# Performance work log

Hardware: AMD Instinct MI355X
Metric: run time of the kernel (lower is better)

Reference implementation:

```python
import jax, jax.numpy as jnp
import numpy as np

N = 50000          # nodes
E = 800000         # edges (COO)
IN_CH = 128
H1, H2, OUT = 200, 100, 2   # 100*out, 50*out, out with out_channels=2
EPS = 1e-12
DROP_P = 0.1


def setup_inputs() -> dict:
    key = jax.random.key(0)
    ks = jax.random.split(key, 6)
    x = jax.random.normal(ks[0], (N, IN_CH), dtype=jnp.float32)
    edge_index = jax.random.randint(ks[1], (2, E), 0, N)
    W1 = jax.random.normal(ks[2], (IN_CH, H1), dtype=jnp.float32) / np.sqrt(IN_CH)
    W2 = jax.random.normal(ks[3], (H1, H2), dtype=jnp.float32) / np.sqrt(H1)
    W3 = jax.random.normal(ks[4], (H2, OUT), dtype=jnp.float32) / np.sqrt(H2)
    beta1 = jnp.float32(1.0)
    beta2 = jnp.float32(1.0)
    beta3 = jnp.float32(1.0)
    return dict(x=x, edge_index=edge_index, W1=W1, W2=W2, W3=W3,
                beta1=beta1, beta2=beta2, beta3=beta3)


def _agnn_layer(x, W, beta, src, dst):
    # project in -> out channels, then AGNN cosine-attention propagation
    h = x @ W                                               # [N, D]
    hn = h / jnp.maximum(jnp.linalg.norm(h, axis=-1, keepdims=True), EPS)
    a = beta * jnp.sum(hn[src] * hn[dst], axis=-1)          # [E'] edge logits
    amax = jax.ops.segment_max(a, dst, num_segments=N)      # stable segment softmax
    amax = jnp.where(jnp.isfinite(amax), amax, 0.0)
    e = jnp.exp(a - amax[dst])
    denom = jax.ops.segment_sum(e, dst, num_segments=N)
    alpha = e / jnp.maximum(denom[dst], EPS)
    return jax.ops.segment_sum(h[src] * alpha[:, None], dst, num_segments=N)


def _dropout(k, x, p=DROP_P):
    keep = jax.random.bernoulli(k, 1.0 - p, x.shape)
    return jnp.where(keep, x / (1.0 - p), 0.0)


def reference(x, edge_index, W1, W2, W3, beta1, beta2, beta3):
    src, dst = edge_index[0], edge_index[1]
    loop = jnp.arange(N)                                    # self-loops (AGNNConv default)
    src = jnp.concatenate([src, loop])
    dst = jnp.concatenate([dst, loop])
    k1, k2 = jax.random.split(jax.random.key(42))
    h = jax.nn.relu(_agnn_layer(x, W1, beta1, src, dst))
    h = _dropout(k1, h)
    h = jax.nn.relu(_agnn_layer(h, W2, beta2, src, dst))
    h = _dropout(k2, h)
    h = jax.nn.relu(_agnn_layer(h, W3, beta3, src, dst))
    return h
```

## Files before the change

kernel.cpp:

```cpp
#include <hip/hip_runtime.h>
#include <hip/hip_bf16.h>

#define NN 50000
#define NE 800000
#define TE 850000
#define EPSN 1e-12f


#define H_OFF    0ull
#define A_OFF    40000000ull
#define H3_OFF   80000000ull
#define RINV_OFF 80400000ull
#define OFFS_OFF 80600000ull
#define DEG_OFF  80800016ull
#define CURS_OFF 81000016ull
#define ESRC_OFF 81200016ull
#define CHNK_OFF 84600016ull

__host__ __device__ inline void tf20(unsigned k0, unsigned k1, unsigned& x0, unsigned& x1) {
  unsigned ks2 = k0 ^ k1 ^ 0x1BD11BDAu;
  x0 += k0; x1 += k1;
#define TFR(r) { x0 += x1; x1 = ((x1 << (r)) | (x1 >> (32 - (r)))) ^ x0; }
  TFR(13) TFR(15) TFR(26) TFR(6)
  x0 += k1;  x1 += ks2 + 1u;
  TFR(17) TFR(29) TFR(16) TFR(24)
  x0 += ks2; x1 += k0 + 2u;
  TFR(13) TFR(15) TFR(26) TFR(6)
  x0 += k0;  x1 += k1 + 3u;
  TFR(17) TFR(29) TFR(16) TFR(24)
  x0 += k1;  x1 += ks2 + 4u;
  TFR(13) TFR(15) TFR(26) TFR(6)
  x0 += ks2; x1 += k0 + 5u;
#undef TFR
}

__device__ __forceinline__ float dropf(float val, unsigned k0, unsigned k1, unsigned i) {
  unsigned x0 = 0u, x1 = i;
  tf20(k0, k1, x0, x1);
  unsigned bits = x0 ^ x1;
  float u = __uint_as_float((bits >> 9) | 0x3F800000u) - 1.0f;
  return (u < 0.9f) ? val * (1.0f / 0.9f) : 0.0f;
}

__device__ __forceinline__ float wave_sum(float x) {
  x += __shfl_xor(x, 32); x += __shfl_xor(x, 16); x += __shfl_xor(x, 8);
  x += __shfl_xor(x, 4);  x += __shfl_xor(x, 2);  x += __shfl_xor(x, 1);
  return x;
}

__global__ __launch_bounds__(256) void csr_zero_kernel(int* __restrict__ p, int n) {
  int stride = gridDim.x * 256;
  for (int i = blockIdx.x * 256 + threadIdx.x; i < n; i += stride) p[i] = 0;
}

__global__ __launch_bounds__(256) void csr_hist_kernel(const int* __restrict__ ei, int* __restrict__ deg) {
  int e = blockIdx.x * 256 + threadIdx.x;
  if (e >= TE) return;
  int d = (e < NE) ? ei[NE + e] : (e - NE);
  atomicAdd(&deg[d], 1);
}

__global__ __launch_bounds__(256) void csr_scan1_kernel(const int* __restrict__ deg,
                                                        int* __restrict__ offs,
                                                        int* __restrict__ chunk) {
  __shared__ int lds[8];
  int t = threadIdx.x;
  int base = blockIdx.x * 1024 + t * 4;
  int d[4];
#pragma unroll
  for (int j = 0; j < 4; j++) d[j] = (base + j < NN) ? deg[base + j] : 0;
  int ts = d[0] + d[1] + d[2] + d[3];
  int lane = t & 63, wave = t >> 6;
  int inc = ts;
#pragma unroll
  for (int sh = 1; sh < 64; sh <<= 1) { int u = __shfl_up(inc, sh); if (lane >= sh) inc += u; }
  if (lane == 63) lds[wave] = inc;
  __syncthreads();
  if (t == 0) { int s = 0; for (int w = 0; w < 4; w++) { int x = lds[w]; lds[w] = s; s += x; } lds[4] = s; }
  __syncthreads();
  int p = lds[wave] + inc - ts;
#pragma unroll
  for (int j = 0; j < 4; j++) { if (base + j < NN) offs[base + j] = p; p += d[j]; }
  if (t == 255) chunk[blockIdx.x] = lds[4];
}

__global__ __launch_bounds__(64) void csr_scan2_kernel(int* __restrict__ chunk) {
  int t = threadIdx.x;
  int v = (t < 49) ? chunk[t] : 0;
  int inc = v;
#pragma unroll
  for (int sh = 1; sh < 64; sh <<= 1) { int u = __shfl_up(inc, sh); if (t >= sh) inc += u; }
  if (t < 49) chunk[t] = inc - v;
}

__global__ __launch_bounds__(256) void csr_scan3_kernel(int* __restrict__ offs,
                                                        const int* __restrict__ chunk,
                                                        int* __restrict__ curs) {
  int i = blockIdx.x * 256 + threadIdx.x;
  if (i < NN) {
    int val = offs[i] + chunk[i >> 10];
    offs[i] = val;
    curs[i] = val;
  }
  if (i == 0) offs[NN] = TE;
}

__global__ __launch_bounds__(256) void csr_scatter_kernel(const int* __restrict__ ei,
                                                          int* __restrict__ curs,
                                                          int* __restrict__ esrc) {
  int e = blockIdx.x * 256 + threadIdx.x;
  if (e >= TE) return;
  int s, d;
  if (e < NE) { s = ei[e]; d = ei[NE + e]; } else { s = d = e - NE; }
  int pos = atomicAdd(&curs[d], 1);
  esrc[pos] = s;
}

template<int K, int KT, int NLP, int N>
__device__ __forceinline__ void gemm_body(const float* __restrict__ A,
                                          const float* __restrict__ W,
                                          float* __restrict__ H,
                                          float* __restrict__ RINV, int M) {
  constexpr int CPT = NLP / 4, KTP = KT + 1, NV = N / 4, QV = CPT / 4;
  __shared__ float As[128 * KTP];
  __shared__ float Ws[KT * NLP];
  const float4* A4 = (const float4*)A;
  const float4* W4 = (const float4*)W;
  const float4* Ws4 = (const float4*)Ws;

  int t = threadIdx.x, rgrp = t >> 2, cg = t & 3;
  int row0 = blockIdx.x * 128;
  float acc0[CPT], acc1[CPT];
#pragma unroll
  for (int j = 0; j < CPT; j++) { acc0[j] = 0.f; acc1[j] = 0.f; }

  for (int k0 = 0; k0 < K; k0 += KT) {
    __syncthreads();
    for (int idx = t; idx < 128 * (KT / 4); idx += 256) {
      int r = idx / (KT / 4), cq = idx - r * (KT / 4);
      int gr = row0 + r;
      float4 v = (gr < M) ? A4[(size_t)gr * (K / 4) + (k0 / 4) + cq]
                          : make_float4(0.f, 0.f, 0.f, 0.f);
      float* dst = &As[r * KTP + cq * 4];
      dst[0] = v.x; dst[1] = v.y; dst[2] = v.z; dst[3] = v.w;
    }
    for (int idx = t; idx < KT * NV; idx += 256) {
      int kk = idx / NV, cq = idx - kk * NV;
      *(float4*)&Ws[kk * NLP + cq * 4] = W4[(size_t)(k0 + kk) * NV + cq];
    }
    if (NLP > N) {
      for (int idx = t; idx < KT * ((NLP - N) / 4); idx += 256) {
        int kk = idx / ((NLP - N) / 4), cq = idx - kk * ((NLP - N) / 4);
        *(float4*)&Ws[kk * NLP + N + cq * 4] = make_float4(0.f, 0.f, 0.f, 0.f);
      }
    }
    __syncthreads();
#pragma unroll
    for (int kk = 0; kk < KT; kk++) {
      float a0 = As[(rgrp * 2) * KTP + kk];
      float a1 = As[(rgrp * 2 + 1) * KTP + kk];
#pragma unroll
      for (int q = 0; q < QV; q++) {
        float4 wv = Ws4[(kk * NLP + cg * CPT) / 4 + q];
        acc0[q * 4 + 0] = fmaf(a0, wv.x, acc0[q * 4 + 0]);
        acc0[q * 4 + 1] = fmaf(a0, wv.y, acc0[q * 4 + 1]);
        acc0[q * 4 + 2] = fmaf(a0, wv.z, acc0[q * 4 + 2]);
        acc0[q * 4 + 3] = fmaf(a0, wv.w, acc0[q * 4 + 3]);
        acc1[q * 4 + 0] = fmaf(a1, wv.x, acc1[q * 4 + 0]);
        acc1[q * 4 + 1] = fmaf(a1, wv.y, acc1[q * 4 + 1]);
        acc1[q * 4 + 2] = fmaf(a1, wv.z, acc1[q * 4 + 2]);
        acc1[q * 4 + 3] = fmaf(a1, wv.w, acc1[q * 4 + 3]);
      }
    }
  }

  int r0 = row0 + rgrp * 2;
#pragma unroll
  for (int rr = 0; rr < 2; rr++) {
    int gr = r0 + rr;
    const float* acc = rr ? acc1 : acc0;
    float ss = 0.f;
#pragma unroll
    for (int j = 0; j < CPT; j++) {
      float v = acc[j];
      ss += v * v;
      int c = cg * CPT + j;
      if (gr < M && c < N) H[(size_t)gr * N + c] = v;
    }
    ss += __shfl_xor(ss, 1); ss += __shfl_xor(ss, 2);
    if (cg == 0 && gr < M) RINV[gr] = 1.0f / fmaxf(sqrtf(ss), EPSN);
  }
}

__global__ __launch_bounds__(256) void gemm1_kernel(const float* A, const float* W,
                                                    float* H, float* RINV, int M) {
  gemm_body<128, 32, 208, 200>(A, W, H, RINV, M);
}
__global__ __launch_bounds__(256) void gemm2_kernel(const float* A, const float* W,
                                                    float* H, float* RINV, int M) {
  gemm_body<200, 40, 112, 100>(A, W, H, RINV, M);
}

template<int D, int VEC, bool DROP>
__device__ __forceinline__ void attn_body(const float* __restrict__ H,
                                          const float* __restrict__ RINV,
                                          const int* __restrict__ OFFS,
                                          const int* __restrict__ ESRC,
                                          const float* __restrict__ BETA,
                                          float* __restrict__ OUT,
                                          unsigned k0, unsigned k1) {
  constexpr int NL = D / VEC;
  int v = blockIdx.x * 4 + (threadIdx.x >> 6);
  int lane = threadIdx.x & 63;
  bool act = lane < NL;
  const float* hrow = H + (size_t)v * D + lane * VEC;
  float hd[VEC];
#pragma unroll
  for (int j = 0; j < VEC; j++) hd[j] = 0.f;
  if (act) {
    if (VEC == 4) { float4 tv = *(const float4*)hrow; hd[0] = tv.x; hd[1] = tv.y; hd[2] = tv.z; hd[3] = tv.w; }
    else          { float2 tv = *(const float2*)hrow; hd[0] = tv.x; hd[1] = tv.y; }
  }
  float bd = BETA[0] * RINV[v];
  int e0 = OFFS[v], e1 = OFFS[v + 1];

  float s = 0.0f;
  float acc[VEC];
#pragma unroll
  for (int j = 0; j < VEC; j++) acc[j] = 0.0f;

  int idx = e0;
  for (; idx + 4 <= e1; idx += 4) {
    int   u[4];
    float r[4], dt[4], hs[4][VEC];
#pragma unroll
    for (int m = 0; m < 4; m++) u[m] = ESRC[idx + m];
#pragma unroll
    for (int m = 0; m < 4; m++) r[m] = RINV[u[m]];
#pragma unroll
    for (int m = 0; m < 4; m++) {
      const float* p = H + (size_t)u[m] * D + lane * VEC;
#pragma unroll
      for (int j = 0; j < VEC; j++) hs[m][j] = 0.f;
      if (act) {
        if (VEC == 4) { float4 a = *(const float4*)p; hs[m][0] = a.x; hs[m][1] = a.y; hs[m][2] = a.z; hs[m][3] = a.w; }
        else          { float2 a = *(const float2*)p; hs[m][0] = a.x; hs[m][1] = a.y; }
      }
    }
#pragma unroll
    for (int m = 0; m < 4; m++) {
      float d = 0.f;
#pragma unroll
      for (int j = 0; j < VEC; j++) d = fmaf(hd[j], hs[m][j], d);
      dt[m] = wave_sum(d);
    }
#pragma unroll
    for (int m = 0; m < 4; m++) {
      float w = __expf(bd * dt[m] * r[m]);
      s += w;
#pragma unroll
      for (int j = 0; j < VEC; j++) acc[j] = fmaf(w, hs[m][j], acc[j]);
    }
  }
  for (; idx < e1; ++idx) {
    int u0 = ESRC[idx];
    float r0 = RINV[u0];
    const float* p0 = H + (size_t)u0 * D + lane * VEC;
    float h0[VEC];
#pragma unroll
    for (int j = 0; j < VEC; j++) h0[j] = 0.f;
    if (act) {
      if (VEC == 4) { float4 a = *(const float4*)p0; h0[0] = a.x; h0[1] = a.y; h0[2] = a.z; h0[3] = a.w; }
      else          { float2 a = *(const float2*)p0; h0[0] = a.x; h0[1] = a.y; }
    }
    float d0 = 0.f;
#pragma unroll
    for (int j = 0; j < VEC; j++) d0 = fmaf(hd[j], h0[j], d0);
    d0 = wave_sum(d0);
    float w0 = __expf(bd * d0 * r0);
    s += w0;
#pragma unroll
    for (int j = 0; j < VEC; j++) acc[j] = fmaf(w0, h0[j], acc[j]);
  }

  float rs = 1.0f / fmaxf(s, EPSN);
  if (act) {
    float o[VEC];
#pragma unroll
    for (int j = 0; j < VEC; j++) {
      float val = acc[j] * rs;
      val = (val <= 0.0f) ? 0.0f : val;
      if (DROP) val = dropf(val, k0, k1, (unsigned)(v * D + lane * VEC + j));
      o[j] = val;
    }
    float* orow = OUT + (size_t)v * D + lane * VEC;
    if (VEC == 4) *(float4*)orow = make_float4(o[0], o[1], o[2], o[3]);
    else          *(float2*)orow = make_float2(o[0], o[1]);
  }
}

__global__ __launch_bounds__(256) void attn1_kernel(const float* H, const float* RINV,
                                                    const int* OFFS, const int* ESRC,
                                                    const float* BETA, float* OUT,
                                                    unsigned k0, unsigned k1) {
  attn_body<200, 4, true>(H, RINV, OFFS, ESRC, BETA, OUT, k0, k1);
}
__global__ __launch_bounds__(256) void attn2_kernel(const float* H, const float* RINV,
                                                    const int* OFFS, const int* ESRC,
                                                    const float* BETA, float* OUT,
                                                    unsigned k0, unsigned k1) {
  attn_body<100, 2, true>(H, RINV, OFFS, ESRC, BETA, OUT, k0, k1);
}

__global__ __launch_bounds__(256) void gemm3_kernel(const float* __restrict__ A2,
                                                    const float* __restrict__ W3,
                                                    float* __restrict__ H3,
                                                    float* __restrict__ RINV) {
  __shared__ float w3s[200];
  for (int i = threadIdx.x; i < 200; i += 256) w3s[i] = W3[i];
  __syncthreads();
  int v = blockIdx.x * 256 + threadIdx.x;
  if (v >= NN) return;
  const float* row = A2 + (size_t)v * 100;
  float o0 = 0.f, o1 = 0.f;
#pragma unroll 4
  for (int k = 0; k < 100; k++) {
    float x = row[k];
    o0 = fmaf(x, w3s[2 * k], o0);
    o1 = fmaf(x, w3s[2 * k + 1], o1);
  }
  H3[2 * v] = o0; H3[2 * v + 1] = o1;
  RINV[v] = 1.0f / fmaxf(sqrtf(o0 * o0 + o1 * o1), EPSN);
}

__global__ __launch_bounds__(256) void attn3_kernel(const float* __restrict__ H3,
                                                    const float* __restrict__ RINV,
                                                    const int* __restrict__ OFFS,
                                                    const int* __restrict__ ESRC,
                                                    const float* __restrict__ BETA,
                                                    float* __restrict__ out) {
  int v = blockIdx.x * 4 + (threadIdx.x >> 6);
  int lane = threadIdx.x & 63;
  float bd = BETA[0] * RINV[v];
  float h0 = H3[2 * v], h1 = H3[2 * v + 1];
  int e0 = OFFS[v], e1 = OFFS[v + 1];
  float s = 0.f, a0 = 0.f, a1 = 0.f;
  for (int idx = e0 + lane; idx < e1; idx += 64) {
    int u = ESRC[idx];
    float s0 = H3[2 * u], s1 = H3[2 * u + 1];
    float w = __expf(bd * (h0 * s0 + h1 * s1) * RINV[u]);
    s += w; a0 = fmaf(w, s0, a0); a1 = fmaf(w, s1, a1);
  }
  s = wave_sum(s); a0 = wave_sum(a0); a1 = wave_sum(a1);
  if (lane == 0) {
    float rs = 1.0f / fmaxf(s, EPSN);
    float o0 = a0 * rs, o1 = a1 * rs;
    out[2 * v]     = (o0 <= 0.0f) ? 0.0f : o0;
    out[2 * v + 1] = (o1 <= 0.0f) ? 0.0f : o1;
  }
}

extern "C" void kernel_launch(void* const* d_in, const int* in_sizes, int n_in,
                              void* d_out, int out_size, void* d_ws, size_t ws_size,
                              hipStream_t stream) {
  const float* X  = (const float*)d_in[0];
  const int*   EI = (const int*)d_in[1];
  const float* W1 = (const float*)d_in[2];
  const float* W2 = (const float*)d_in[3];
  const float* W3 = (const float*)d_in[4];
  const float* B1 = (const float*)d_in[5];
  const float* B2 = (const float*)d_in[6];
  const float* B3 = (const float*)d_in[7];

  char* ws = (char*)d_ws;
  float* H    = (float*)(ws + H_OFF);
  float* A    = (float*)(ws + A_OFF);
  float* H3   = (float*)(ws + H3_OFF);
  float* RINV = (float*)(ws + RINV_OFF);
  int* OFFS   = (int*)(ws + OFFS_OFF);
  int* DEG    = (int*)(ws + DEG_OFF);
  int* CURS   = (int*)(ws + CURS_OFF);
  int* ESRC   = (int*)(ws + ESRC_OFF);
  int* CHNK   = (int*)(ws + CHNK_OFF);

  unsigned k1a = 0u, k1b = 0u; tf20(0u, 42u, k1a, k1b);
  unsigned k2a = 0u, k2b = 1u; tf20(0u, 42u, k2a, k2b);

  csr_zero_kernel<<<64, 256, 0, stream>>>(DEG, NN);
  csr_hist_kernel<<<(TE + 255) / 256, 256, 0, stream>>>(EI, DEG);
  csr_scan1_kernel<<<49, 256, 0, stream>>>(DEG, OFFS, CHNK);
  csr_scan2_kernel<<<1, 64, 0, stream>>>(CHNK);
  csr_scan3_kernel<<<196, 256, 0, stream>>>(OFFS, CHNK, CURS);
  csr_scatter_kernel<<<(TE + 255) / 256, 256, 0, stream>>>(EI, CURS, ESRC);

  const int gb = (NN + 127) / 128;
  const int ab = NN / 4;

  gemm1_kernel<<<gb, 256, 0, stream>>>(X, W1, H, RINV, NN);
  attn1_kernel<<<ab, 256, 0, stream>>>(H, RINV, OFFS, ESRC, B1, A, k1a, k1b);
  gemm2_kernel<<<gb, 256, 0, stream>>>(A, W2, H, RINV, NN);
  attn2_kernel<<<ab, 256, 0, stream>>>(H, RINV, OFFS, ESRC, B2, A, k2a, k2b);
  gemm3_kernel<<<(NN + 255) / 256, 256, 0, stream>>>(A, W3, H3, RINV);
  attn3_kernel<<<ab, 256, 0, stream>>>(H3, RINV, OFFS, ESRC, B3, (float*)d_out);
}
```

Before: 546.4 us.

## Fuse layer-3 projection into attn2 epilogue and halve GEMM row tile

The layer-2 attention kernel now multiplies its post-ReLU/dropout output row by W3 with a wave reduction. It writes only the 2-wide H3 and its inverse norm into a separate RINV3 buffer. This removes the standalone gemm3 kernel and the write and re-read of the 50000x100 activation. Separately, the shared GEMM body drops from 128 to 64 rows per block, with one row per thread instead of two. That lowers register pressure and doubles the block count, at the cost of loading each W tile into LDS for fewer rows.

```diff
diff --git a/kernel.cpp b/kernel.cpp
--- a/kernel.cpp
+++ b/kernel.cpp
@@ -16,6 +16,7 @@
 #define CURS_OFF 81000016ull
 #define ESRC_OFF 81200016ull
 #define CHNK_OFF 84600016ull
+#define RINV3_OFF 84600272ull
 
 __host__ __device__ inline void tf20(unsigned k0, unsigned k1, unsigned& x0, unsigned& x1) {
   unsigned ks2 = k0 ^ k1 ^ 0x1BD11BDAu;
@@ -122,21 +123,21 @@
                                           float* __restrict__ H,
                                           float* __restrict__ RINV, int M) {
   constexpr int CPT = NLP / 4, KTP = KT + 1, NV = N / 4, QV = CPT / 4;
-  __shared__ float As[128 * KTP];
+  __shared__ float As[64 * KTP];
   __shared__ float Ws[KT * NLP];
   const float4* A4 = (const float4*)A;
   const float4* W4 = (const float4*)W;
   const float4* Ws4 = (const float4*)Ws;
 
   int t = threadIdx.x, rgrp = t >> 2, cg = t & 3;
-  int row0 = blockIdx.x * 128;
-  float acc0[CPT], acc1[CPT];
-#pragma unroll
-  for (int j = 0; j < CPT; j++) { acc0[j] = 0.f; acc1[j] = 0.f; }
+  int row0 = blockIdx.x * 64;
+  float acc[CPT];
+#pragma unroll
+  for (int j = 0; j < CPT; j++) acc[j] = 0.f;
 
   for (int k0 = 0; k0 < K; k0 += KT) {
     __syncthreads();
-    for (int idx = t; idx < 128 * (KT / 4); idx += 256) {
+    for (int idx = t; idx < 64 * (KT / 4); idx += 256) {
       int r = idx / (KT / 4), cq = idx - r * (KT / 4);
       int gr = row0 + r;
       float4 v = (gr < M) ? A4[(size_t)gr * (K / 4) + (k0 / 4) + cq]
@@ -157,39 +158,29 @@
     __syncthreads();
 #pragma unroll
     for (int kk = 0; kk < KT; kk++) {
-      float a0 = As[(rgrp * 2) * KTP + kk];
-      float a1 = As[(rgrp * 2 + 1) * KTP + kk];
+      float a0 = As[rgrp * KTP + kk];
 #pragma unroll
       for (int q = 0; q < QV; q++) {
         float4 wv = Ws4[(kk * NLP + cg * CPT) / 4 + q];
-        acc0[q * 4 + 0] = fmaf(a0, wv.x, acc0[q * 4 + 0]);
-        acc0[q * 4 + 1] = fmaf(a0, wv.y, acc0[q * 4 + 1]);
-        acc0[q * 4 + 2] = fmaf(a0, wv.z, acc0[q * 4 + 2]);
-        acc0[q * 4 + 3] = fmaf(a0, wv.w, acc0[q * 4 + 3]);
-        acc1[q * 4 + 0] = fmaf(a1, wv.x, acc1[q * 4 + 0]);
-        acc1[q * 4 + 1] = fmaf(a1, wv.y, acc1[q * 4 + 1]);
-        acc1[q * 4 + 2] = fmaf(a1, wv.z, acc1[q * 4 + 2]);
-        acc1[q * 4 + 3] = fmaf(a1, wv.w, acc1[q * 4 + 3]);
+        acc[q * 4 + 0] = fmaf(a0, wv.x, acc[q * 4 + 0]);
+        acc[q * 4 + 1] = fmaf(a0, wv.y, acc[q * 4 + 1]);
+        acc[q * 4 + 2] = fmaf(a0, wv.z, acc[q * 4 + 2]);
+        acc[q * 4 + 3] = fmaf(a0, wv.w, acc[q * 4 + 3]);
       }
     }
   }
 
-  int r0 = row0 + rgrp * 2;
-#pragma unroll
-  for (int rr = 0; rr < 2; rr++) {
-    int gr = r0 + rr;
-    const float* acc = rr ? acc1 : acc0;
-    float ss = 0.f;
-#pragma unroll
-    for (int j = 0; j < CPT; j++) {
-      float v = acc[j];
-      ss += v * v;
-      int c = cg * CPT + j;
-      if (gr < M && c < N) H[(size_t)gr * N + c] = v;
-    }
-    ss += __shfl_xor(ss, 1); ss += __shfl_xor(ss, 2);
-    if (cg == 0 && gr < M) RINV[gr] = 1.0f / fmaxf(sqrtf(ss), EPSN);
-  }
+  int gr = row0 + rgrp;
+  float ss = 0.f;
+#pragma unroll
+  for (int j = 0; j < CPT; j++) {
+    float v = acc[j];
+    ss += v * v;
+    int c = cg * CPT + j;
+    if (gr < M && c < N) H[(size_t)gr * N + c] = v;
+  }
+  ss += __shfl_xor(ss, 1); ss += __shfl_xor(ss, 2);
+  if (cg == 0 && gr < M) RINV[gr] = 1.0f / fmaxf(sqrtf(ss), EPSN);
 }
 
 __global__ __launch_bounds__(256) void gemm1_kernel(const float* A, const float* W,
@@ -201,13 +192,16 @@
   gemm_body<200, 40, 112, 100>(A, W, H, RINV, M);
 }
 
-template<int D, int VEC, bool DROP>
+template<int D, int VEC, bool DROP, bool G3FUSE>
 __device__ __forceinline__ void attn_body(const float* __restrict__ H,
                                           const float* __restrict__ RINV,
                                           const int* __restrict__ OFFS,
                                           const int* __restrict__ ESRC,
                                           const float* __restrict__ BETA,
                                           float* __restrict__ OUT,
+                                          const float* __restrict__ W3g,
+                                          float* __restrict__ H3,
+                                          float* __restrict__ RINVO,
                                           unsigned k0, unsigned k1) {
   constexpr int NL = D / VEC;
   int v = blockIdx.x * 4 + (threadIdx.x >> 6);
@@ -284,15 +278,28 @@
   }
 
   float rs = 1.0f / fmaxf(s, EPSN);
-  if (act) {
-    float o[VEC];
-#pragma unroll
-    for (int j = 0; j < VEC; j++) {
-      float val = acc[j] * rs;
-      val = (val <= 0.0f) ? 0.0f : val;
-      if (DROP) val = dropf(val, k0, k1, (unsigned)(v * D + lane * VEC + j));
-      o[j] = val;
-    }
+  float o[VEC];
+#pragma unroll
+  for (int j = 0; j < VEC; j++) {
+    float val = acc[j] * rs;
+    val = (val <= 0.0f) ? 0.0f : val;
+    if (DROP) val = dropf(val, k0, k1, (unsigned)(v * D + lane * VEC + j));
+    o[j] = act ? val : 0.0f;
+  }
+  if (G3FUSE) {
+    float p0 = 0.f, p1 = 0.f;
+    if (act) {
+      float w00 = W3g[4 * lane], w01 = W3g[4 * lane + 1];
+      float w10 = W3g[4 * lane + 2], w11 = W3g[4 * lane + 3];
+      p0 = o[0] * w00 + o[1] * w10;
+      p1 = o[0] * w01 + o[1] * w11;
+    }
+    p0 = wave_sum(p0); p1 = wave_sum(p1);
+    if (lane == 0) {
+      H3[2 * v] = p0; H3[2 * v + 1] = p1;
+      RINVO[v] = 1.0f / fmaxf(sqrtf(p0 * p0 + p1 * p1), EPSN);
+    }
+  } else if (act) {
     float* orow = OUT + (size_t)v * D + lane * VEC;
     if (VEC == 4) *(float4*)orow = make_float4(o[0], o[1], o[2], o[3]);
     else          *(float2*)orow = make_float2(o[0], o[1]);
@@ -303,52 +310,32 @@
                                                     const int* OFFS, const int* ESRC,
                                                     const float* BETA, float* OUT,
                                                     unsigned k0, unsigned k1) {
-  attn_body<200, 4, true>(H, RINV, OFFS, ESRC, BETA, OUT, k0, k1);
-}
-__global__ __launch_bounds__(256) void attn2_kernel(const float* H, const float* RINV,
-                                                    const int* OFFS, const int* ESRC,
-                                                    const float* BETA, float* OUT,
-                                                    unsigned k0, unsigned k1) {
-  attn_body<100, 2, true>(H, RINV, OFFS, ESRC, BETA, OUT, k0, k1);
-}
-
-__global__ __launch_bounds__(256) void gemm3_kernel(const float* __restrict__ A2,
-                                                    const float* __restrict__ W3,
-                                                    float* __restrict__ H3,
-                                                    float* __restrict__ RINV) {
-  __shared__ float w3s[200];
-  for (int i = threadIdx.x; i < 200; i += 256) w3s[i] = W3[i];
-  __syncthreads();
-  int v = blockIdx.x * 256 + threadIdx.x;
-  if (v >= NN) return;
-  const float* row = A2 + (size_t)v * 100;
-  float o0 = 0.f, o1 = 0.f;
-#pragma unroll 4
-  for (int k = 0; k < 100; k++) {
-    float x = row[k];
-    o0 = fmaf(x, w3s[2 * k], o0);
-    o1 = fmaf(x, w3s[2 * k + 1], o1);
-  }
-  H3[2 * v] = o0; H3[2 * v + 1] = o1;
-  RINV[v] = 1.0f / fmaxf(sqrtf(o0 * o0 + o1 * o1), EPSN);
+  attn_body<200, 4, true, false>(H, RINV, OFFS, ESRC, BETA, OUT, nullptr, nullptr, nullptr, k0, k1);
+}
+__global__ __launch_bounds__(256) void attn2g3_kernel(const float* H, const float* RINV,
+                                                      const int* OFFS, const int* ESRC,
+                                                      const float* BETA, const float* W3g,
+                                                      float* H3, float* RINV3,
+                                                      unsigned k0, unsigned k1) {
+  attn_body<100, 2, true, true>(H, RINV, OFFS, ESRC, BETA, nullptr, W3g, H3, RINV3, k0, k1);
 }
 
 __global__ __launch_bounds__(256) void attn3_kernel(const float* __restrict__ H3,
-                                                    const float* __restrict__ RINV,
+                                                    const float* __restrict__ RINV3,
                                                     const int* __restrict__ OFFS,
                                                     const int* __restrict__ ESRC,
                                                     const float* __restrict__ BETA,
                                                     float* __restrict__ out) {
   int v = blockIdx.x * 4 + (threadIdx.x >> 6);
   int lane = threadIdx.x & 63;
-  float bd = BETA[0] * RINV[v];
+  float bd = BETA[0] * RINV3[v];
   float h0 = H3[2 * v], h1 = H3[2 * v + 1];
   int e0 = OFFS[v], e1 = OFFS[v + 1];
   float s = 0.f, a0 = 0.f, a1 = 0.f;
   for (int idx = e0 + lane; idx < e1; idx += 64) {
     int u = ESRC[idx];
     float s0 = H3[2 * u], s1 = H3[2 * u + 1];
-    float w = __expf(bd * (h0 * s0 + h1 * s1) * RINV[u]);
+    float w = __expf(bd * (h0 * s0 + h1 * s1) * RINV3[u]);
     s += w; a0 = fmaf(w, s0, a0); a1 = fmaf(w, s1, a1);
   }
   s = wave_sum(s); a0 = wave_sum(a0); a1 = wave_sum(a1);
@@ -373,15 +360,16 @@
   const float* B3 = (const float*)d_in[7];
 
   char* ws = (char*)d_ws;
-  float* H    = (float*)(ws + H_OFF);
-  float* A    = (float*)(ws + A_OFF);
-  float* H3   = (float*)(ws + H3_OFF);
-  float* RINV = (float*)(ws + RINV_OFF);
-  int* OFFS   = (int*)(ws + OFFS_OFF);
-  int* DEG    = (int*)(ws + DEG_OFF);
-  int* CURS   = (int*)(ws + CURS_OFF);
-  int* ESRC   = (int*)(ws + ESRC_OFF);
-  int* CHNK   = (int*)(ws + CHNK_OFF);
+  float* H     = (float*)(ws + H_OFF);
+  float* A     = (float*)(ws + A_OFF);
+  float* H3    = (float*)(ws + H3_OFF);
+  float* RINV  = (float*)(ws + RINV_OFF);
+  float* RINV3 = (float*)(ws + RINV3_OFF);
+  int* OFFS    = (int*)(ws + OFFS_OFF);
+  int* DEG     = (int*)(ws + DEG_OFF);
+  int* CURS    = (int*)(ws + CURS_OFF);
+  int* ESRC    = (int*)(ws + ESRC_OFF);
+  int* CHNK    = (int*)(ws + CHNK_OFF);
 
   unsigned k1a = 0u, k1b = 0u; tf20(0u, 42u, k1a, k1b);
   unsigned k2a = 0u, k2b = 1u; tf20(0u, 42u, k2a, k2b);
@@ -393,13 +381,12 @@
   csr_scan3_kernel<<<196, 256, 0, stream>>>(OFFS, CHNK, CURS);
   csr_scatter_kernel<<<(TE + 255) / 256, 256, 0, stream>>>(EI, CURS, ESRC);
 
-  const int gb = (NN + 127) / 128;
+  const int gb = (NN + 63) / 64;
   const int ab = NN / 4;
 
   gemm1_kernel<<<gb, 256, 0, stream>>>(X, W1, H, RINV, NN);
   attn1_kernel<<<ab, 256, 0, stream>>>(H, RINV, OFFS, ESRC, B1, A, k1a, k1b);
   gemm2_kernel<<<gb, 256, 0, stream>>>(A, W2, H, RINV, NN);
-  attn2_kernel<<<ab, 256, 0, stream>>>(H, RINV, OFFS, ESRC, B2, A, k2a, k2b);
-  gemm3_kernel<<<(NN + 255) / 256, 256, 0, stream>>>(A, W3, H3, RINV);
-  attn3_kernel<<<ab, 256, 0, stream>>>(H3, RINV, OFFS, ESRC, B3, (float*)d_out);
-}
+  attn2g3_kernel<<<ab, 256, 0, stream>>>(H, RINV, OFFS, ESRC, B2, W3, H3, RINV3, k2a, k2b);
+  attn3_kernel<<<ab, 256, 0, stream>>>(H3, RINV3, OFFS, ESRC, B3, (float*)d_out);
+}
```

Result: slower. 596.6 us (+9.2%).
